# Performance work log

Measured on AMD Instinct MI355X. Metric: run time of the kernel, lower is better.

## Reference

```python
import jax, jax.numpy as jnp
from jax import lax
import numpy as np

HIDDEN = 256

def _lstm_layer(x_tbf, w_ih, w_hh, b_ih, b_hh):
    # x_tbf: [T, B, F]; w_ih: [4H, F]; w_hh: [4H, H]
    B = x_tbf.shape[1]
    # precompute input projections for all timesteps: [T, B, 4H]
    xg = jnp.einsum('tbf,gf->tbg', x_tbf, w_ih) + b_ih + b_hh
    def step(carry, xg_t):
        h, c = carry
        g = xg_t + h @ w_hh.T  # [B, 4H]
        i, f, gg, o = jnp.split(g, 4, axis=-1)  # torch gate order: i, f, g, o
        i = jax.nn.sigmoid(i)
        f = jax.nn.sigmoid(f)
        gg = jnp.tanh(gg)
        o = jax.nn.sigmoid(o)
        c = f * c + i * gg
        h = o * jnp.tanh(c)
        return (h, c), h
    init = (jnp.zeros((B, HIDDEN), x_tbf.dtype), jnp.zeros((B, HIDDEN), x_tbf.dtype))
    _, hs = lax.scan(step, init, xg)
    return hs  # [T, B, H]


def setup_inputs() -> dict:
    key = jax.random.key(0)
    ks = jax.random.split(key, 16)
    B, T, F_IN, NSPK = 64, 1024, 40, 1251
    s = 1.0 / np.sqrt(HIDDEN)
    def u(k, shape):
        return jax.random.uniform(k, shape, jnp.float32, -s, s)
    inp = {'x': jax.random.normal(ks[0], (B, T, F_IN), jnp.float32)}
    in_dims = [F_IN, HIDDEN, HIDDEN]
    ki = 1
    for l in range(3):
        inp[f'w_ih{l}'] = u(ks[ki], (4 * HIDDEN, in_dims[l])); ki += 1
        inp[f'w_hh{l}'] = u(ks[ki], (4 * HIDDEN, HIDDEN)); ki += 1
        inp[f'b_ih{l}'] = u(ks[ki], (4 * HIDDEN,)); ki += 1
        inp[f'b_hh{l}'] = u(ks[ki], (4 * HIDDEN,)); ki += 1
    inp['w_lin'] = u(ks[13], (NSPK, HIDDEN))
    inp['b_lin'] = u(ks[14], (NSPK,))
    return inp


def reference(x, w_ih0, w_hh0, b_ih0, b_hh0, w_ih1, w_hh1, b_ih1, b_hh1,
              w_ih2, w_hh2, b_ih2, b_hh2, w_lin, b_lin):
    # x: [B, T, F] (batch_first). Run 3 stacked LSTM layers.
    h = jnp.transpose(x, (1, 0, 2))  # [T, B, F]
    params = [(w_ih0, w_hh0, b_ih0, b_hh0),
              (w_ih1, w_hh1, b_ih1, b_hh1),
              (w_ih2, w_hh2, b_ih2, b_hh2)]
    for w_ih, w_hh, b_ih, b_hh in params:
        h = _lstm_layer(h, w_ih, w_hh, b_ih, b_hh)
    lstm_out = jnp.transpose(h, (1, 0, 2))  # [B, T, H]
    # Faithful to original: lstm_out[-1] selects the LAST BATCH element -> [T, H]
    last = lstm_out[-1]
    logits = last @ w_lin.T + b_lin  # [T, NSPK]
    return jax.nn.log_softmax(logits, axis=1)
```

## Files before the change

### kernel.cpp

```cpp
#include <hip/hip_runtime.h>

#define HID 256
#define T_STEPS 1024
#define F_IN 40
#define NSPK 1251
#define NCHUNK 8
#define NBLOCKS (3 * NCHUNK)
#define K2_THREADS 512

#define HBUF_WORDS (3 * 1025 * 256)
#define H2F_OFF_BYTES ((size_t)HBUF_WORDS * 8)

__device__ __forceinline__ float fast_sig(float v) {
    return __builtin_amdgcn_rcpf(1.f + __expf(-v));
}
__device__ __forceinline__ float fast_tanh(float v) {
    return 2.f * __builtin_amdgcn_rcpf(1.f + __expf(-2.f * v)) - 1.f;
}

__global__ void k0_init(unsigned long long* __restrict__ hbuf) {
    int tid = threadIdx.x;
    if (tid < 3 * HID) {
        int l = tid / HID, k = tid % HID;
        hbuf[(size_t)(l * 1025 + 0) * HID + k] = 0ull;
    }
}

__global__ __launch_bounds__(K2_THREADS) void k2_lstm(
    const float* __restrict__ x,
    const float* __restrict__ w_ih0, const float* __restrict__ w_hh0,
    const float* __restrict__ b_ih0, const float* __restrict__ b_hh0,
    const float* __restrict__ w_ih1, const float* __restrict__ w_hh1,
    const float* __restrict__ b_ih1, const float* __restrict__ b_hh1,
    const float* __restrict__ w_ih2, const float* __restrict__ w_hh2,
    const float* __restrict__ b_ih2, const float* __restrict__ b_hh2,
    unsigned long long* __restrict__ hbuf, float* __restrict__ h2f)
{
    const int bid = blockIdx.x;
    const int layer = bid / NCHUNK;
    const int g     = bid % NCHUNK;
    const int tid   = threadIdx.x;
    const int row_idx = tid >> 2;
    const int seg     = tid & 3;
    const int q  = row_idx >> 5;
    const int jj = row_idx & 31;
    const int r  = q * 256 + g * 32 + jj;

    const float* wih = (layer == 0) ? w_ih0 : (layer == 1) ? w_ih1 : w_ih2;
    const float* whh = (layer == 0) ? w_hh0 : (layer == 1) ? w_hh1 : w_hh2;
    const float* bih = (layer == 0) ? b_ih0 : (layer == 1) ? b_ih1 : b_ih2;
    const float* bhh = (layer == 0) ? b_hh0 : (layer == 1) ? b_hh1 : b_hh2;

    __shared__ float lds_in[512];
    __shared__ float lds_gate[128];

    float w[128];
    const int rot4 = 2 * seg;
    if (seg >= 2) {
        const float4* src = (const float4*)(whh + r * HID + (seg - 2) * 128);
        #pragma unroll
        for (int k4 = 0; k4 < 32; k4++) {
            float4 v = src[(k4 + rot4) & 31];
            w[k4 * 4 + 0] = v.x; w[k4 * 4 + 1] = v.y;
            w[k4 * 4 + 2] = v.z; w[k4 * 4 + 3] = v.w;
        }
    } else if (layer > 0) {
        const float4* src = (const float4*)(wih + r * HID + seg * 128);
        #pragma unroll
        for (int k4 = 0; k4 < 32; k4++) {
            float4 v = src[(k4 + rot4) & 31];
            w[k4 * 4 + 0] = v.x; w[k4 * 4 + 1] = v.y;
            w[k4 * 4 + 2] = v.z; w[k4 * 4 + 3] = v.w;
        }
    } else {
        #pragma unroll
        for (int k = 0; k < 128; k++) w[k] = 0.f;
        if (seg == 0) {
            for (int k = 0; k < F_IN; k++) w[k] = w_ih0[r * F_IN + k];
        }
    }
    float bias = (seg == 0) ? (bih[r] + bhh[r]) : 0.f;

    for (int i = tid; i < 512; i += K2_THREADS) lds_in[i] = 0.f;
    __syncthreads();

    const float* x63 = x + 63 * T_STEPS * F_IN;
    const unsigned long long* h_prev_layer = hbuf + (size_t)(layer - 1) * 1025 * HID;
    unsigned long long* h_own              = hbuf + (size_t)layer * 1025 * HID;

    float c_state = 0.f;

    for (int t = 0; t < T_STEPS; t++) {
        if (tid < 256) {
            const unsigned long long* p = h_own + (size_t)t * HID + tid;
            unsigned long long v;
            do {
                v = __hip_atomic_load(p, __ATOMIC_RELAXED, __HIP_MEMORY_SCOPE_AGENT);
            } while ((unsigned)(v >> 32) != (unsigned)t);
            lds_in[256 + tid] = __uint_as_float((unsigned)v);
        } else if (layer > 0) {
            const unsigned long long* p = h_prev_layer + (size_t)(t + 1) * HID + (tid - 256);
            unsigned long long v;
            do {
                v = __hip_atomic_load(p, __ATOMIC_RELAXED, __HIP_MEMORY_SCOPE_AGENT);
            } while ((unsigned)(v >> 32) != (unsigned)(t + 1));
            lds_in[tid - 256] = __uint_as_float((unsigned)v);
        } else if (tid < 256 + 10) {
            ((float4*)lds_in)[tid - 256] = ((const float4*)(x63 + t * F_IN))[tid - 256];
        }
        __syncthreads();

        float acc = 0.f;
        const float* in = lds_in + seg * 128;
        const int rot = seg * 8;
        #pragma unroll
        for (int k4 = 0; k4 < 32; k4++) {
            int base = (k4 * 4 + rot) & 127;
            acc += w[k4 * 4 + 0] * in[base + 0];
            acc += w[k4 * 4 + 1] * in[base + 1];
            acc += w[k4 * 4 + 2] * in[base + 2];
            acc += w[k4 * 4 + 3] * in[base + 3];
        }
        acc += __shfl_xor(acc, 1, 64);
        acc += __shfl_xor(acc, 2, 64);
        if (seg == 0) lds_gate[row_idx] = acc + bias;
        __syncthreads();

        if (tid < 32) {
            float gi = lds_gate[tid];
            float gf = lds_gate[32 + tid];
            float gg = lds_gate[64 + tid];
            float go = lds_gate[96 + tid];
            float si = fast_sig(gi);
            float sf = fast_sig(gf);
            float so = fast_sig(go);
            c_state = sf * c_state + si * fast_tanh(gg);
            float hv = so * fast_tanh(c_state);
            unsigned long long word =
                ((unsigned long long)(unsigned)(t + 1) << 32) | (unsigned long long)__float_as_uint(hv);
            __hip_atomic_store(h_own + (size_t)(t + 1) * HID + g * 32 + tid, word,
                               __ATOMIC_RELAXED, __HIP_MEMORY_SCOPE_AGENT);
            if (layer == 2) h2f[(size_t)t * HID + g * 32 + tid] = hv;
        }
    }
}

#define BM 64
#define BN 64
#define BK 32
__global__ __launch_bounds__(256) void k3_logits(
    const float* __restrict__ A, const float* __restrict__ w_lin,
    const float* __restrict__ b_lin, float* __restrict__ out)
{
    int m0 = blockIdx.x * BM;
    int n0 = blockIdx.y * BN;
    int tid = threadIdx.x;
    __shared__ float As[BM][BK + 1];
    __shared__ float Bs[BN][BK + 1];
    float accv[4][4] = {};
    int tx = tid % 16, ty = tid / 16;

    for (int k0 = 0; k0 < HID; k0 += BK) {
        int row = tid / 4;
        int kq  = (tid % 4) * 8;
        {
            const float4* src = (const float4*)(A + (m0 + row) * HID + k0 + kq);
            float4 v0 = src[0], v1 = src[1];
            As[row][kq + 0] = v0.x; As[row][kq + 1] = v0.y; As[row][kq + 2] = v0.z; As[row][kq + 3] = v0.w;
            As[row][kq + 4] = v1.x; As[row][kq + 5] = v1.y; As[row][kq + 6] = v1.z; As[row][kq + 7] = v1.w;
        }
        {
            int n = n0 + row;
            float4 v0 = make_float4(0.f, 0.f, 0.f, 0.f), v1 = v0;
            if (n < NSPK) {
                const float4* src = (const float4*)(w_lin + n * HID + k0 + kq);
                v0 = src[0]; v1 = src[1];
            }
            Bs[row][kq + 0] = v0.x; Bs[row][kq + 1] = v0.y; Bs[row][kq + 2] = v0.z; Bs[row][kq + 3] = v0.w;
            Bs[row][kq + 4] = v1.x; Bs[row][kq + 5] = v1.y; Bs[row][kq + 6] = v1.z; Bs[row][kq + 7] = v1.w;
        }
        __syncthreads();
        #pragma unroll
        for (int kk = 0; kk < BK; kk++) {
            float a0 = As[ty * 4 + 0][kk], a1 = As[ty * 4 + 1][kk];
            float a2 = As[ty * 4 + 2][kk], a3 = As[ty * 4 + 3][kk];
            float b0 = Bs[tx * 4 + 0][kk], b1 = Bs[tx * 4 + 1][kk];
            float b2 = Bs[tx * 4 + 2][kk], b3 = Bs[tx * 4 + 3][kk];
            accv[0][0] += a0 * b0; accv[0][1] += a0 * b1; accv[0][2] += a0 * b2; accv[0][3] += a0 * b3;
            accv[1][0] += a1 * b0; accv[1][1] += a1 * b1; accv[1][2] += a1 * b2; accv[1][3] += a1 * b3;
            accv[2][0] += a2 * b0; accv[2][1] += a2 * b1; accv[2][2] += a2 * b2; accv[2][3] += a2 * b3;
            accv[3][0] += a3 * b0; accv[3][1] += a3 * b1; accv[3][2] += a3 * b2; accv[3][3] += a3 * b3;
        }
        __syncthreads();
    }
    #pragma unroll
    for (int i = 0; i < 4; i++) {
        int m = m0 + ty * 4 + i;
        #pragma unroll
        for (int j = 0; j < 4; j++) {
            int n = n0 + tx * 4 + j;
            if (n < NSPK) out[(size_t)m * NSPK + n] = accv[i][j] + b_lin[n];
        }
    }
}

__global__ __launch_bounds__(256) void k4_logsoftmax(float* __restrict__ out)
{
    int t = blockIdx.x;
    float* row = out + (size_t)t * NSPK;
    int tid = threadIdx.x;
    __shared__ float red[8];
    float vals[5];
    float lmax = -1e30f;
    #pragma unroll
    for (int k = 0; k < 5; k++) {
        int n = tid + k * 256;
        vals[k] = (n < NSPK) ? row[n] : -1e30f;
        lmax = fmaxf(lmax, vals[k]);
    }
    #pragma unroll
    for (int m = 1; m < 64; m <<= 1) lmax = fmaxf(lmax, __shfl_xor(lmax, m, 64));
    int wave = tid >> 6;
    if ((tid & 63) == 0) red[wave] = lmax;
    __syncthreads();
    float gmax = fmaxf(fmaxf(red[0], red[1]), fmaxf(red[2], red[3]));
    float lsum = 0.f;
    #pragma unroll
    for (int k = 0; k < 5; k++) {
        int n = tid + k * 256;
        if (n < NSPK) lsum += __expf(vals[k] - gmax);
    }
    #pragma unroll
    for (int m = 1; m < 64; m <<= 1) lsum += __shfl_xor(lsum, m, 64);
    if ((tid & 63) == 0) red[4 + wave] = lsum;
    __syncthreads();
    float lse = logf(red[4] + red[5] + red[6] + red[7]) + gmax;
    #pragma unroll
    for (int k = 0; k < 5; k++) {
        int n = tid + k * 256;
        if (n < NSPK) row[n] = vals[k] - lse;
    }
}

extern "C" void kernel_launch(void* const* d_in, const int* in_sizes, int n_in,
                              void* d_out, int out_size, void* d_ws, size_t ws_size,
                              hipStream_t stream) {
    const float* x     = (const float*)d_in[0];
    const float* w_ih0 = (const float*)d_in[1];
    const float* w_hh0 = (const float*)d_in[2];
    const float* b_ih0 = (const float*)d_in[3];
    const float* b_hh0 = (const float*)d_in[4];
    const float* w_ih1 = (const float*)d_in[5];
    const float* w_hh1 = (const float*)d_in[6];
    const float* b_ih1 = (const float*)d_in[7];
    const float* b_hh1 = (const float*)d_in[8];
    const float* w_ih2 = (const float*)d_in[9];
    const float* w_hh2 = (const float*)d_in[10];
    const float* b_ih2 = (const float*)d_in[11];
    const float* b_hh2 = (const float*)d_in[12];
    const float* w_lin = (const float*)d_in[13];
    const float* b_lin = (const float*)d_in[14];

    unsigned long long* hbuf = (unsigned long long*)d_ws;
    float* h2f = (float*)((char*)d_ws + H2F_OFF_BYTES);
    float* out = (float*)d_out;

    k0_init<<<1, 1024, 0, stream>>>(hbuf);
    k2_lstm<<<NBLOCKS, K2_THREADS, 0, stream>>>(
        x, w_ih0, w_hh0, b_ih0, b_hh0,
        w_ih1, w_hh1, b_ih1, b_hh1,
        w_ih2, w_hh2, b_ih2, b_hh2,
        hbuf, h2f);
    k3_logits<<<dim3(16, 20), 256, 0, stream>>>(h2f, w_lin, b_lin, out);
    k4_logsoftmax<<<T_STEPS, 256, 0, stream>>>(out);
}
```

Baseline: 1.995 ms.

## Remap LSTM gate rows so gates combine via shuffles, double-buffer LDS inputs

Rows are remapped so the four gates (i,f,g,o) for one hidden unit sit in the same 16-lane group, and they are combined with cross-lane shuffles instead of an LDS gate buffer plus a second __syncthreads per timestep. The LDS input buffer is double-buffered by timestep parity. Each block writes its own h slice straight into the next buffer rather than polling global memory for it, and layer 0 prefetches the next x row. Four partial accumulators also break the FMA dependency chain. The goal is a shorter serial per-timestep critical path, at the cost of more shuffles and the gate math running in 32 scattered lanes.

```diff
diff --git a/kernel.cpp b/kernel.cpp
--- a/kernel.cpp
+++ b/kernel.cpp
@@ -40,19 +40,17 @@
     const int layer = bid / NCHUNK;
     const int g     = bid % NCHUNK;
     const int tid   = threadIdx.x;
-    const int row_idx = tid >> 2;
-    const int seg     = tid & 3;
-    const int q  = row_idx >> 5;
-    const int jj = row_idx & 31;
-    const int r  = q * 256 + g * 32 + jj;
+    const int seg = tid & 3;
+    const int q   = (tid >> 2) & 3;
+    const int j   = tid >> 4;
+    const int r   = q * 256 + g * 32 + j;
 
     const float* wih = (layer == 0) ? w_ih0 : (layer == 1) ? w_ih1 : w_ih2;
     const float* whh = (layer == 0) ? w_hh0 : (layer == 1) ? w_hh1 : w_hh2;
     const float* bih = (layer == 0) ? b_ih0 : (layer == 1) ? b_ih1 : b_ih2;
     const float* bhh = (layer == 0) ? b_hh0 : (layer == 1) ? b_hh1 : b_hh2;
 
-    __shared__ float lds_in[512];
-    __shared__ float lds_gate[128];
+    __shared__ float lds_sh[1024];
 
     float w[128];
     const int rot4 = 2 * seg;
@@ -81,7 +79,7 @@
     }
     float bias = (seg == 0) ? (bih[r] + bhh[r]) : 0.f;
 
-    for (int i = tid; i < 512; i += K2_THREADS) lds_in[i] = 0.f;
+    for (int i = tid; i < 1024; i += K2_THREADS) lds_sh[i] = 0.f;
     __syncthreads();
 
     const float* x63 = x + 63 * T_STEPS * F_IN;
@@ -89,58 +87,68 @@
     unsigned long long* h_own              = hbuf + (size_t)layer * 1025 * HID;
 
     float c_state = 0.f;
+    const bool is_upd = ((tid & 15) == 0);
 
     for (int t = 0; t < T_STEPS; t++) {
+        float* buf  = lds_sh + ((t & 1) << 9);
+        float* bufn = lds_sh + (((t + 1) & 1) << 9);
+
         if (tid < 256) {
-            const unsigned long long* p = h_own + (size_t)t * HID + tid;
-            unsigned long long v;
-            do {
-                v = __hip_atomic_load(p, __ATOMIC_RELAXED, __HIP_MEMORY_SCOPE_AGENT);
-            } while ((unsigned)(v >> 32) != (unsigned)t);
-            lds_in[256 + tid] = __uint_as_float((unsigned)v);
+            const int k = tid;
+            if ((k >> 5) != g) {
+                const unsigned long long* p = h_own + (size_t)t * HID + k;
+                unsigned long long v;
+                do {
+                    v = __hip_atomic_load(p, __ATOMIC_RELAXED, __HIP_MEMORY_SCOPE_AGENT);
+                } while ((unsigned)(v >> 32) != (unsigned)t);
+                buf[256 + k] = __uint_as_float((unsigned)v);
+            }
         } else if (layer > 0) {
             const unsigned long long* p = h_prev_layer + (size_t)(t + 1) * HID + (tid - 256);
             unsigned long long v;
             do {
                 v = __hip_atomic_load(p, __ATOMIC_RELAXED, __HIP_MEMORY_SCOPE_AGENT);
             } while ((unsigned)(v >> 32) != (unsigned)(t + 1));
-            lds_in[tid - 256] = __uint_as_float((unsigned)v);
-        } else if (tid < 256 + 10) {
-            ((float4*)lds_in)[tid - 256] = ((const float4*)(x63 + t * F_IN))[tid - 256];
+            buf[tid - 256] = __uint_as_float((unsigned)v);
+        } else if (tid < 256 + 10 && t == 0) {
+            ((float4*)buf)[tid - 256] = ((const float4*)(x63))[tid - 256];
         }
         __syncthreads();
 
-        float acc = 0.f;
-        const float* in = lds_in + seg * 128;
+        if (layer == 0 && tid >= 256 && tid < 256 + 10 && t + 1 < T_STEPS) {
+            ((float4*)bufn)[tid - 256] = ((const float4*)(x63 + (t + 1) * F_IN))[tid - 256];
+        }
+
+        float a0 = 0.f, a1 = 0.f, a2 = 0.f, a3 = 0.f;
+        const float* in = buf + seg * 128;
         const int rot = seg * 8;
         #pragma unroll
         for (int k4 = 0; k4 < 32; k4++) {
             int base = (k4 * 4 + rot) & 127;
-            acc += w[k4 * 4 + 0] * in[base + 0];
-            acc += w[k4 * 4 + 1] * in[base + 1];
-            acc += w[k4 * 4 + 2] * in[base + 2];
-            acc += w[k4 * 4 + 3] * in[base + 3];
-        }
+            a0 += w[k4 * 4 + 0] * in[base + 0];
+            a1 += w[k4 * 4 + 1] * in[base + 1];
+            a2 += w[k4 * 4 + 2] * in[base + 2];
+            a3 += w[k4 * 4 + 3] * in[base + 3];
+        }
+        float acc = (a0 + a1) + (a2 + a3) + bias;
         acc += __shfl_xor(acc, 1, 64);
         acc += __shfl_xor(acc, 2, 64);
-        if (seg == 0) lds_gate[row_idx] = acc + bias;
-        __syncthreads();
-
-        if (tid < 32) {
-            float gi = lds_gate[tid];
-            float gf = lds_gate[32 + tid];
-            float gg = lds_gate[64 + tid];
-            float go = lds_gate[96 + tid];
-            float si = fast_sig(gi);
-            float sf = fast_sig(gf);
-            float so = fast_sig(go);
-            c_state = sf * c_state + si * fast_tanh(gg);
+        float vf = __shfl_xor(acc, 4, 64);
+        float vg = __shfl_xor(acc, 8, 64);
+        float vo = __shfl_xor(vf, 8, 64);
+
+        if (is_upd) {
+            float si = fast_sig(acc);
+            float sf = fast_sig(vf);
+            float so = fast_sig(vo);
+            c_state = sf * c_state + si * fast_tanh(vg);
             float hv = so * fast_tanh(c_state);
             unsigned long long word =
                 ((unsigned long long)(unsigned)(t + 1) << 32) | (unsigned long long)__float_as_uint(hv);
-            __hip_atomic_store(h_own + (size_t)(t + 1) * HID + g * 32 + tid, word,
+            __hip_atomic_store(h_own + (size_t)(t + 1) * HID + g * 32 + j, word,
                                __ATOMIC_RELAXED, __HIP_MEMORY_SCOPE_AGENT);
-            if (layer == 2) h2f[(size_t)t * HID + g * 32 + tid] = hv;
+            bufn[256 + g * 32 + j] = hv;
+            if (layer == 2) h2f[(size_t)t * HID + g * 32 + j] = hv;
         }
     }
 }
```

After: 2.289 ms. 1.15x slower.

## Restructure LSTM step: per-thread 4-gate accumulation, local h reuse, x prefetch

Applied to the files above, without the earlier changes.

Reorganizes work so each group of 16 threads owns one hidden unit and accumulates all four gates over a 32-wide slice of the concatenated input, reducing with shuffles. The gate nonlinearities and cell update then run in the reducing lane, which removes the separate gate LDS stage. The block's own h slice is read from LDS instead of spinning on global atomics. Layer-0 x rows are prefetched one step ahead. The cost is more shuffle rounds per step and a different register layout, which may raise register pressure.

```diff
diff --git a/kernel.cpp b/kernel.cpp
--- a/kernel.cpp
+++ b/kernel.cpp
@@ -40,102 +40,114 @@
     const int layer = bid / NCHUNK;
     const int g     = bid % NCHUNK;
     const int tid   = threadIdx.x;
-    const int row_idx = tid >> 2;
-    const int seg     = tid & 3;
-    const int q  = row_idx >> 5;
-    const int jj = row_idx & 31;
-    const int r  = q * 256 + g * 32 + jj;
+    const int seg = tid & 15;
+    const int j   = tid >> 4;
+    const int jg  = g * 32 + j;
 
     const float* wih = (layer == 0) ? w_ih0 : (layer == 1) ? w_ih1 : w_ih2;
     const float* whh = (layer == 0) ? w_hh0 : (layer == 1) ? w_hh1 : w_hh2;
     const float* bih = (layer == 0) ? b_ih0 : (layer == 1) ? b_ih1 : b_ih2;
     const float* bhh = (layer == 0) ? b_hh0 : (layer == 1) ? b_hh1 : b_hh2;
 
-    __shared__ float lds_in[512];
-    __shared__ float lds_gate[128];
-
-    float w[128];
-    const int rot4 = 2 * seg;
-    if (seg >= 2) {
-        const float4* src = (const float4*)(whh + r * HID + (seg - 2) * 128);
-        #pragma unroll
-        for (int k4 = 0; k4 < 32; k4++) {
-            float4 v = src[(k4 + rot4) & 31];
-            w[k4 * 4 + 0] = v.x; w[k4 * 4 + 1] = v.y;
-            w[k4 * 4 + 2] = v.z; w[k4 * 4 + 3] = v.w;
-        }
-    } else if (layer > 0) {
-        const float4* src = (const float4*)(wih + r * HID + seg * 128);
-        #pragma unroll
-        for (int k4 = 0; k4 < 32; k4++) {
-            float4 v = src[(k4 + rot4) & 31];
-            w[k4 * 4 + 0] = v.x; w[k4 * 4 + 1] = v.y;
-            w[k4 * 4 + 2] = v.z; w[k4 * 4 + 3] = v.w;
-        }
-    } else {
-        #pragma unroll
-        for (int k = 0; k < 128; k++) w[k] = 0.f;
-        if (seg == 0) {
-            for (int k = 0; k < F_IN; k++) w[k] = w_ih0[r * F_IN + k];
-        }
-    }
-    float bias = (seg == 0) ? (bih[r] + bhh[r]) : 0.f;
-
-    for (int i = tid; i < 512; i += K2_THREADS) lds_in[i] = 0.f;
+    __shared__ float buf[512];
+    __shared__ float hv_lds[32];
+
+    float w[4][32];
+    float bb[4];
+    const int rot = (2 * seg) & 31;
+    #pragma unroll
+    for (int q = 0; q < 4; q++) {
+        const int r = q * 256 + jg;
+        bb[q] = bih[r] + bhh[r];
+        if (layer > 0) {
+            #pragma unroll
+            for (int i = 0; i < 32; i++) {
+                int k = seg * 32 + ((i + rot) & 31);
+                w[q][i] = (k < HID) ? wih[(size_t)r * HID + k]
+                                    : whh[(size_t)r * HID + (k - HID)];
+            }
+        } else {
+            #pragma unroll
+            for (int i = 0; i < 32; i++) {
+                int k = seg * 32 + ((i + rot) & 31);
+                w[q][i] = (k < F_IN) ? w_ih0[r * F_IN + k]
+                        : (k >= HID) ? whh[(size_t)r * HID + (k - HID)]
+                                     : 0.f;
+            }
+        }
+    }
+
+    for (int i = tid; i < 512; i += K2_THREADS) buf[i] = 0.f;
+    if (tid < 32) hv_lds[tid] = 0.f;
     __syncthreads();
 
     const float* x63 = x + 63 * T_STEPS * F_IN;
     const unsigned long long* h_prev_layer = hbuf + (size_t)(layer - 1) * 1025 * HID;
     unsigned long long* h_own              = hbuf + (size_t)layer * 1025 * HID;
 
+    float4 px = make_float4(0.f, 0.f, 0.f, 0.f);
+    if (layer == 0 && tid >= 256 && tid < 256 + 10)
+        px = ((const float4*)x63)[tid - 256];
+
     float c_state = 0.f;
 
     for (int t = 0; t < T_STEPS; t++) {
         if (tid < 256) {
-            const unsigned long long* p = h_own + (size_t)t * HID + tid;
-            unsigned long long v;
-            do {
-                v = __hip_atomic_load(p, __ATOMIC_RELAXED, __HIP_MEMORY_SCOPE_AGENT);
-            } while ((unsigned)(v >> 32) != (unsigned)t);
-            lds_in[256 + tid] = __uint_as_float((unsigned)v);
+            if ((tid >> 5) == g) {
+                buf[256 + tid] = hv_lds[tid & 31];
+            } else {
+                const unsigned long long* p = h_own + (size_t)t * HID + tid;
+                unsigned long long v;
+                do {
+                    v = __hip_atomic_load(p, __ATOMIC_RELAXED, __HIP_MEMORY_SCOPE_AGENT);
+                } while ((unsigned)(v >> 32) != (unsigned)t);
+                buf[256 + tid] = __uint_as_float((unsigned)v);
+            }
         } else if (layer > 0) {
             const unsigned long long* p = h_prev_layer + (size_t)(t + 1) * HID + (tid - 256);
             unsigned long long v;
             do {
                 v = __hip_atomic_load(p, __ATOMIC_RELAXED, __HIP_MEMORY_SCOPE_AGENT);
             } while ((unsigned)(v >> 32) != (unsigned)(t + 1));
-            lds_in[tid - 256] = __uint_as_float((unsigned)v);
+            buf[tid - 256] = __uint_as_float((unsigned)v);
         } else if (tid < 256 + 10) {
-            ((float4*)lds_in)[tid - 256] = ((const float4*)(x63 + t * F_IN))[tid - 256];
-        }
-        __syncthreads();
-
-        float acc = 0.f;
-        const float* in = lds_in + seg * 128;
-        const int rot = seg * 8;
-        #pragma unroll
-        for (int k4 = 0; k4 < 32; k4++) {
-            int base = (k4 * 4 + rot) & 127;
-            acc += w[k4 * 4 + 0] * in[base + 0];
-            acc += w[k4 * 4 + 1] * in[base + 1];
-            acc += w[k4 * 4 + 2] * in[base + 2];
-            acc += w[k4 * 4 + 3] * in[base + 3];
-        }
-        acc += __shfl_xor(acc, 1, 64);
-        acc += __shfl_xor(acc, 2, 64);
-        if (seg == 0) lds_gate[row_idx] = acc + bias;
+            ((float4*)buf)[tid - 256] = px;
+            if (t + 1 < T_STEPS)
+                px = ((const float4*)(x63 + (t + 1) * F_IN))[tid - 256];
+        }
+        __syncthreads();
+
+        float a0 = 0.f, a1 = 0.f, a2 = 0.f, a3 = 0.f;
+        const float* bufs = buf + seg * 32;
+        #pragma unroll
+        for (int i = 0; i < 32; i++) {
+            float f = bufs[(i + rot) & 31];
+            a0 += w[0][i] * f;
+            a1 += w[1][i] * f;
+            a2 += w[2][i] * f;
+            a3 += w[3][i] * f;
+        }
+        #pragma unroll
+        for (int m = 1; m < 16; m <<= 1) {
+            a0 += __shfl_xor(a0, m, 64);
+            a1 += __shfl_xor(a1, m, 64);
+            a2 += __shfl_xor(a2, m, 64);
+            a3 += __shfl_xor(a3, m, 64);
+        }
+
+        if (seg == 0) {
+            float si = fast_sig(a0 + bb[0]);
+            float sf = fast_sig(a1 + bb[1]);
+            float gg = fast_tanh(a2 + bb[2]);
+            float so = fast_sig(a3 + bb[3]);
+            c_state = sf * c_state + si * gg;
+            float hv = so * fast_tanh(c_state);
+            hv_lds[j] = hv;
+        }
         __syncthreads();
 
         if (tid < 32) {
-            float gi = lds_gate[tid];
-            float gf = lds_gate[32 + tid];
-            float gg = lds_gate[64 + tid];
-            float go = lds_gate[96 + tid];
-            float si = fast_sig(gi);
-            float sf = fast_sig(gf);
-            float so = fast_sig(go);
-            c_state = sf * c_state + si * fast_tanh(gg);
-            float hv = so * fast_tanh(c_state);
+            float hv = hv_lds[tid];
             unsigned long long word =
                 ((unsigned long long)(unsigned)(t + 1) << 32) | (unsigned long long)__float_as_uint(hv);
             __hip_atomic_store(h_own + (size_t)(t + 1) * HID + g * 32 + tid, word,
```

Result: no change. 1.972 ms (-1.2%).
